# Optimization experiments

Hardware: AMD Instinct MI355X
Metric: run time of the kernel (lower is better)

## Reference

```python
import jax, jax.numpy as jnp
import numpy as np

H = 100  # hidden_size
D = 300  # input/output feature dim (hardcoded in module)
T = 32768  # number of timesteps


def _lstm_layer(x_seq, W_ih, W_hh, b_ih, b_hh):
    """Single LSTM layer over time. x_seq: [T, H_in]. PyTorch gate order i,f,g,o."""
    Hh = W_hh.shape[1]
    b = b_ih + b_hh
    # precompute input projection for all timesteps (removes per-step GEMM)
    x_proj = x_seq @ W_ih.T + b  # [T, 4H]

    def step(carry, xp_t):
        h, c = carry
        gates = xp_t + h @ W_hh.T  # [4H]
        i, f, g, o = jnp.split(gates, 4, axis=-1)
        c = jax.nn.sigmoid(f) * c + jax.nn.sigmoid(i) * jnp.tanh(g)
        h = jax.nn.sigmoid(o) * jnp.tanh(c)
        return (h, c), h

    h0 = jnp.zeros((Hh,), x_seq.dtype)
    c0 = jnp.zeros((Hh,), x_seq.dtype)
    (h_T, c_T), hs = jax.lax.scan(step, (h0, c0), x_proj)
    return hs, h_T, c_T


def setup_inputs() -> dict:
    key = jax.random.key(0)
    ks = jax.random.split(key, 14)
    s = 0.08
    return {
        "inputs": jax.random.normal(ks[0], (T, D), jnp.float32),
        "W_inp": jax.random.normal(ks[1], (H, D), jnp.float32) * s,
        "b_inp": jax.random.normal(ks[2], (H,), jnp.float32) * s,
        "W_ih_l0": jax.random.normal(ks[3], (4 * H, H), jnp.float32) * s,
        "W_hh_l0": jax.random.normal(ks[4], (4 * H, H), jnp.float32) * s,
        "b_ih_l0": jax.random.normal(ks[5], (4 * H,), jnp.float32) * s,
        "b_hh_l0": jax.random.normal(ks[6], (4 * H,), jnp.float32) * s,
        "W_ih_l1": jax.random.normal(ks[7], (4 * H, H), jnp.float32) * s,
        "W_hh_l1": jax.random.normal(ks[8], (4 * H, H), jnp.float32) * s,
        "b_ih_l1": jax.random.normal(ks[9], (4 * H,), jnp.float32) * s,
        "b_hh_l1": jax.random.normal(ks[10], (4 * H,), jnp.float32) * s,
        "W_out": jax.random.normal(ks[11], (D, H), jnp.float32) * s,
        "b_out": jax.random.normal(ks[12], (D,), jnp.float32) * s,
    }


def reference(inputs, W_inp, b_inp, W_ih_l0, W_hh_l0, b_ih_l0, b_hh_l0,
              W_ih_l1, W_hh_l1, b_ih_l1, b_hh_l1, W_out, b_out):
    # teacher-forced forward (force=True): input projection for all steps at once
    x = inputs @ W_inp.T + b_inp  # [T, H]
    h0_seq, h0_T, c0_T = _lstm_layer(x, W_ih_l0, W_hh_l0, b_ih_l0, b_hh_l0)
    h1_seq, h1_T, c1_T = _lstm_layer(h0_seq, W_ih_l1, W_hh_l1, b_ih_l1, b_hh_l1)
    outputs = h1_seq @ W_out.T + b_out  # [T, D]
    h_n = jnp.stack([h0_T, h1_T])  # [2, H] final hidden per layer
    c_n = jnp.stack([c0_T, c1_T])  # [2, H] final cell per layer
    return outputs, h_n, c_n
```

## Files before the change

kernel.cpp:

```cpp
#include <hip/hip_runtime.h>

#define T_STEPS 32768
#define OUT_BASE 9830400
#define RMASK 16383

typedef _Float16 h2 __attribute__((ext_vector_type(2)));
#define H2BC(f_) __builtin_bit_cast(h2, f_)

#define ALD(p)     __hip_atomic_load((p), __ATOMIC_RELAXED, __HIP_MEMORY_SCOPE_AGENT)
#define AST(p, v)  __hip_atomic_store((p), (v), __ATOMIC_RELAXED, __HIP_MEMORY_SCOPE_AGENT)
#define ASTR(p, v) __hip_atomic_store((p), (v), __ATOMIC_RELEASE, __HIP_MEMORY_SCOPE_AGENT)
#define CFENCE()   asm volatile("" ::: "memory")

__device__ __forceinline__ float fdot2(h2 a, h2 b, float c) {
#if __has_builtin(__builtin_amdgcn_fdot2)
    return __builtin_amdgcn_fdot2(a, b, c, false);
#else
    return c + (float)a.x * (float)b.x + (float)a.y * (float)b.y;
#endif
}

__device__ __forceinline__ float sigf(float x) { return 1.f / (1.f + __expf(-x)); }

__device__ __forceinline__ float tanh_f(float x) {
    float a = fabsf(x);
    float e = __expf(-2.f * a);
    float t = (1.f - e) / (1.f + e);
    return x < 0.f ? -t : t;
}

template <int CTRL>
__device__ __forceinline__ float qperm(float x) {
#if __has_builtin(__builtin_amdgcn_update_dpp)
    return __builtin_bit_cast(
        float, __builtin_amdgcn_update_dpp(0, __builtin_bit_cast(int, x), CTRL, 0xF, 0xF, true));
#else
    return __shfl_xor(x, CTRL == 0xB1 ? 1 : (CTRL == 0x4E ? 2 : 3));
#endif
}

__device__ __forceinline__ void bar_lds() {
    asm volatile("s_waitcnt lgkmcnt(0)\n\ts_barrier" ::: "memory");
}

__device__ __forceinline__ void ldw(h2* w, const float* p) {
#pragma unroll
    for (int k = 0; k < 25; k++) {
        float2 v = ((const float2*)p)[k];
        h2 t; t.x = (_Float16)v.x; t.y = (_Float16)v.y; w[k] = t;
    }
}

__device__ __forceinline__ float2 mv25(const h2* wA, const h2* wB, const char* rec) {
    const float4* hv = (const float4*)rec;
    float pA = 0.f, pB = 0.f;
#pragma unroll
    for (int c = 0; c < 6; c++) {
        float4 v = hv[c];
        pA = fdot2(wA[4 * c + 0], H2BC(v.x), pA); pB = fdot2(wB[4 * c + 0], H2BC(v.x), pB);
        pA = fdot2(wA[4 * c + 1], H2BC(v.y), pA); pB = fdot2(wB[4 * c + 1], H2BC(v.y), pB);
        pA = fdot2(wA[4 * c + 2], H2BC(v.z), pA); pB = fdot2(wB[4 * c + 2], H2BC(v.z), pB);
        pA = fdot2(wA[4 * c + 3], H2BC(v.w), pA); pB = fdot2(wB[4 * c + 3], H2BC(v.w), pB);
    }
    float vl = *(const float*)(rec + 96);
    pA = fdot2(wA[24], H2BC(vl), pA); pB = fdot2(wB[24], H2BC(vl), pB);
    return make_float2(pA, pB);
}

__global__ void k_precomp(const float* __restrict__ W_inp, const float* __restrict__ b_inp,
                          const float* __restrict__ W_ih0, const float* __restrict__ b_ih0,
                          const float* __restrict__ b_hh0,
                          float* __restrict__ Wc, float* __restrict__ bc) {
    int idx = blockIdx.x * 256 + threadIdx.x;
    if (idx < 120000) {
        int r = idx / 300, d = idx % 300;
        float acc = 0.f;
        for (int h = 0; h < 100; h++) acc += W_ih0[r * 100 + h] * W_inp[h * 300 + d];
        Wc[idx] = acc;
    } else if (idx < 120400) {
        int r = idx - 120000;
        float acc = b_ih0[r] + b_hh0[r];
        for (int h = 0; h < 100; h++) acc += W_ih0[r * 100 + h] * b_inp[h];
        bc[r] = acc;
    }
}

__global__ __launch_bounds__(512) void k_xproj(const float* __restrict__ inp,
                                               const float* __restrict__ Wc,
                                               const float* __restrict__ bc,
                                               _Float16* __restrict__ x0p) {
    __shared__ float xs[32 * 300];
    int t0 = blockIdx.x * 32;
    for (int idx = threadIdx.x; idx < 9600; idx += 512) xs[idx] = inp[(size_t)t0 * 300 + idx];
    __syncthreads();
    int j = threadIdx.x;
    if (j < 400) {
        float acc[32];
#pragma unroll
        for (int i = 0; i < 32; i++) acc[i] = 0.f;
        const float4* w4 = (const float4*)(Wc + j * 300);
        const float4* x4 = (const float4*)xs;
        for (int d4 = 0; d4 < 75; d4++) {
            float4 w = w4[d4];
#pragma unroll
            for (int ti = 0; ti < 32; ti++) {
                float4 x = x4[ti * 75 + d4];
                acc[ti] += w.x * x.x + w.y * x.y + w.z * x.z + w.w * x.w;
            }
        }
        float bb = bc[j];
        int dst = (j % 100) * 4 + j / 100;
#pragma unroll
        for (int ti = 0; ti < 32; ti++)
            x0p[(size_t)(t0 + ti) * 400 + dst] = (_Float16)(acc[ti] + bb);
    }
}


#define B0TICK(T_, XR_, P_) do {                                                             \
    if (j < 400) {                                                                           \
        float xc_ = XR_;                                                                     \
        int tn_ = (T_) + 2 < T_STEPS ? (T_) + 2 : T_STEPS - 1;                               \
        XR_ = (float)x0p[(size_t)tn_ * 400 + j];                                             \
        float2 p_ = mv25(wA, wB, (const char*)(lds + (P_) * 112) + hoff);                    \
        float pA_ = p_.x + qperm<0xB1>(p_.x);                                                \
        float pB_ = p_.y + qperm<0xB1>(p_.y);                                                \
        float sv_ = (H ? pB_ : pA_) + xc_;                                                   \
        float nl_ = __builtin_fmaf(sigf(sv_ * s_), s_, addc_);                               \
        float fg_ = qperm<0xB1>(nl_), gg_ = qperm<0x4E>(nl_), og_ = qperm<0x1B>(nl_);        \
        if (q == 0) {                                                                        \
            c0 = fg_ * c0 + nl_ * gg_;                                                       \
            float h0v_ = og_ * tanh_f(c0);                                                   \
            ((_Float16*)(lds + (1 - (P_)) * 112))[hidx] = (_Float16)h0v_;                    \
            if ((T_) == T_STEPS - 1) { outTail[u] = h0v_; outTail[200 + u] = c0; }           \
        }                                                                                    \
    } else if (j >= 448) {                                                                   \
        if (kk < 50 && (T_) >= 1)                                                            \
            AST(&h0seq[(size_t)((T_) - 1) * 50 + kk], (lds + (P_) * 112)[pidx]);             \
        if (kk == 0 && (((T_) & 7) == 7)) ASTR(&flags[0], (unsigned)(T_));                   \
    }                                                                                        \
    bar_lds();                                                                               \
} while (0)

#define B2TICK(T_, ZR_, P_) do {                                                             \
    if (j < 400) {                                                                           \
        float zc_ = ZR_;                                                                     \
        int tn_ = (T_) + 2 < T_STEPS ? (T_) + 2 : T_STEPS - 1;                               \
        ZR_ = ALD(&z1ring[(size_t)(tn_ & RMASK) * 400 + j]);                                 \
        float2 p_ = mv25(wA, wB, (const char*)(lds + (P_) * 112) + hoff);                    \
        float pA_ = p_.x + qperm<0xB1>(p_.x);                                                \
        float pB_ = p_.y + qperm<0xB1>(p_.y);                                                \
        float sv_ = (H ? pB_ : pA_) + zc_;              \
        float nl_ = __builtin_fmaf(sigf(sv_ * s_), s_, addc_);                               \
        float fg_ = qperm<0xB1>(nl_), gg_ = qperm<0x4E>(nl_), og_ = qperm<0x1B>(nl_);        \
        if (q == 0) {                                                                        \
            c1 = fg_ * c1 + nl_ * gg_;                                                       \
            float h1v_ = og_ * tanh_f(c1);                                                   \
            ((_Float16*)(lds + (1 - (P_)) * 112))[hidx] = (_Float16)h1v_;                    \
            h1s[(size_t)(T_) * 100 + u] = h1v_;                                              \
            if ((T_) == T_STEPS - 1) { outTail[100 + u] = h1v_; outTail[300 + u] = c1; }     \
        }                                                                                    \
    } else if (j == 448) {                                                                   \
        int tq_ = (T_) + 3 < T_STEPS ? (T_) + 3 : T_STEPS - 1;                               \
        unsigned need_ = (unsigned)(tq_ >> 4) + 1u;                                          \
        if (zdc < need_) {                                                                   \
            while ((zdc = ALD(&flags[1])) < need_) __builtin_amdgcn_s_sleep(2);              \
            CFENCE();                                                                        \
        }                                                                                    \
        if (((T_) & 255) == 255) ASTR(&flags[2], (unsigned)(T_) + 1u);                       \
    }                                                                                        \
    bar_lds();                                                                               \
} while (0)

__global__ __launch_bounds__(512) __attribute__((amdgpu_waves_per_eu(2, 2)))
void k_scan3(const _Float16* __restrict__ x0p,
             const float* __restrict__ Whh0,
             const float* __restrict__ Wih1,
             const float* __restrict__ Whh1,
             const float* __restrict__ bih1,
             const float* __restrict__ bhh1,
             float* __restrict__ h1s,
             float* __restrict__ outTail,
             unsigned* __restrict__ h0seq,
             float* __restrict__ z1ring,
             unsigned* __restrict__ flags) {
    __shared__ __align__(16) unsigned lds[16 * 56];
    const int j = threadIdx.x;
    const int q = j & 3, u = j >> 2, H = q & 1, gA = (q >> 1) * 2;
    const int hoff = H * 112;
    const int hidx = (u < 50) ? u : 56 + (u - 50);
    const int kk = j - 448;
    const int pidx = (kk < 25) ? kk : kk + 3;
    const float s_ = (q == 2) ? 2.f : 1.f;
    const float addc_ = (q == 2) ? -1.f : 0.f;

    if (blockIdx.x == 0) {
        h2 wA[25], wB[25];
        float xa = 0.f, xb = 0.f, c0 = 0.f;
        if (j < 400) {
            int r0 = gA * 100 + u;
            ldw(wA, Whh0 + r0 * 100 + 50 * H);
            ldw(wB, Whh0 + (r0 + 100) * 100 + 50 * H);
            xa = (float)x0p[j];
            xb = (float)x0p[400 + j];
        }
        if (j < 224) lds[j] = 0u;
        __syncthreads();

        for (int t = 0; t < T_STEPS; t += 2) {
            B0TICK(t, xa, 0);
            B0TICK(t + 1, xb, 1);
        }
        if (j >= 448) {
            if (kk < 50) AST(&h0seq[(size_t)(T_STEPS - 1) * 50 + kk], lds[pidx]);
            if (kk == 0) ASTR(&flags[0], (unsigned)T_STEPS);
        }
    } else if (blockIdx.x == 1) {
        h2 wA[25], wB[25];
        float bz = 0.f;
        if (j < 400) {
            int r0 = gA * 100 + u;
            ldw(wA, Wih1 + r0 * 100 + 50 * H);
            ldw(wB, Wih1 + (r0 + 100) * 100 + 50 * H);
            int ro = q * 100 + u;
            bz = bih1[ro] + bhh1[ro];
        }
        for (int idx = j; idx < 16 * 56; idx += 512) lds[idx] = 0u;
        __syncthreads();

        unsigned fcache = 0, bpc = 0;
        for (int tau = 0; tau < 2048; ++tau) {
            const int t0 = tau * 16;
            while (fcache < (unsigned)(t0 + 16)) {
                fcache = ALD(&flags[0]);
                if (fcache < (unsigned)(t0 + 16)) __builtin_amdgcn_s_sleep(8);
            }
            int lim = t0 + 32 - (RMASK + 1);
            if (lim > 0) {
                while ((int)bpc < lim) {
                    bpc = ALD(&flags[2]);
                    if ((int)bpc < lim) __builtin_amdgcn_s_sleep(8);
                }
            }
            CFENCE();
            for (int g = j; g < 800; g += 512) {
                int tt = g / 50, k = g % 50;
                lds[tt * 56 + ((k < 25) ? k : k + 3)] = ALD(&h0seq[(size_t)t0 * 50 + g]);
            }
            __syncthreads();
            if (j < 400) {
                for (int tt = 0; tt < 16; ++tt) {
                    float2 p = mv25(wA, wB, (const char*)(lds + tt * 56) + hoff);
                    float pA = p.x + qperm<0xB1>(p.x);
                    float pB = p.y + qperm<0xB1>(p.y);
                    AST(&z1ring[(size_t)((t0 + tt) & RMASK) * 400 + j], (H ? pB : pA) + bz);
                }
            }
            __syncthreads();
            if (j == 0) ASTR(&flags[1], (unsigned)(tau + 1));
        }
    } else {
        h2 wA[25], wB[25];
        float za = 0.f, zb = 0.f, c1 = 0.f;
        unsigned zdc = 0;
        if (j < 400) {
            int r0 = gA * 100 + u;
            ldw(wA, Whh1 + r0 * 100 + 50 * H);
            ldw(wB, Whh1 + (r0 + 100) * 100 + 50 * H);
        }
        if (j < 224) lds[j] = 0u;
        __syncthreads();
        if (j == 448) {
            while ((zdc = ALD(&flags[1])) < 1u) __builtin_amdgcn_s_sleep(8);
            CFENCE();
        }
        __syncthreads();
        if (j < 400) {
            za = ALD(&z1ring[j]);
            zb = ALD(&z1ring[400 + j]);
        }

        for (int t = 0; t < T_STEPS; t += 2) {
            B2TICK(t, za, 0);
            B2TICK(t + 1, zb, 1);
        }
    }
}

__global__ __launch_bounds__(320) void k_out(const float* __restrict__ h1s,
                                             const float* __restrict__ Wout,
                                             const float* __restrict__ bout,
                                             float* __restrict__ out) {
    __shared__ float hs[32 * 100];
    int t0 = blockIdx.x * 32;
    for (int idx = threadIdx.x; idx < 3200; idx += 320) hs[idx] = h1s[(size_t)t0 * 100 + idx];
    __syncthreads();
    int d = threadIdx.x;
    if (d < 300) {
        float acc[32];
#pragma unroll
        for (int i = 0; i < 32; i++) acc[i] = 0.f;
        const float4* w4 = (const float4*)(Wout + d * 100);
        const float4* h4 = (const float4*)hs;
        for (int j4 = 0; j4 < 25; j4++) {
            float4 w = w4[j4];
#pragma unroll
            for (int ti = 0; ti < 32; ti++) {
                float4 h = h4[ti * 25 + j4];
                acc[ti] += w.x * h.x + w.y * h.y + w.z * h.z + w.w * h.w;
            }
        }
        float bb = bout[d];
#pragma unroll
        for (int ti = 0; ti < 32; ti++) out[(size_t)(t0 + ti) * 300 + d] = acc[ti] + bb;
    }
}

extern "C" void kernel_launch(void* const* d_in, const int* in_sizes, int n_in,
                              void* d_out, int out_size, void* d_ws, size_t ws_size,
                              hipStream_t stream) {
    const float* inputs = (const float*)d_in[0];
    const float* W_inp  = (const float*)d_in[1];
    const float* b_inp  = (const float*)d_in[2];
    const float* W_ih0  = (const float*)d_in[3];
    const float* W_hh0  = (const float*)d_in[4];
    const float* b_ih0  = (const float*)d_in[5];
    const float* b_hh0  = (const float*)d_in[6];
    const float* W_ih1  = (const float*)d_in[7];
    const float* W_hh1  = (const float*)d_in[8];
    const float* b_ih1  = (const float*)d_in[9];
    const float* b_hh1  = (const float*)d_in[10];
    const float* W_out  = (const float*)d_in[11];
    const float* b_out  = (const float*)d_in[12];
    float* out = (float*)d_out;

    char* ws = (char*)d_ws;
    _Float16* x0p = (_Float16*)ws;
    float* h1s = (float*)(ws + 26214400);
    float* Wc  = (float*)(ws + 26214400 + 13107200);
    float* bc  = Wc + 120000;

    float*    z1ring = out;
    unsigned* h0seq  = (unsigned*)((char*)out + 26214400);
    unsigned* flagsp = (unsigned*)((char*)out + 32768000);
    float*    outTail = out + OUT_BASE;

    hipMemsetAsync(flagsp, 0, 16, stream);
    k_precomp<<<471, 256, 0, stream>>>(W_inp, b_inp, W_ih0, b_ih0, b_hh0, Wc, bc);
    k_xproj<<<1024, 512, 0, stream>>>(inputs, Wc, bc, x0p);

    void* args[] = {(void*)&x0p, (void*)&W_hh0, (void*)&W_ih1, (void*)&W_hh1,
                    (void*)&b_ih1, (void*)&b_hh1, (void*)&h1s, (void*)&outTail,
                    (void*)&h0seq, (void*)&z1ring, (void*)&flagsp};
    hipLaunchCooperativeKernel((void*)k_scan3, dim3(3), dim3(512), args, 0, stream);

    k_out<<<1024, 320, 0, stream>>>(h1s, W_out, b_out, out);
}
```

Before: 20.73 ms.

## Spread recurrent matvec over 800 threads with one gate row per thread

Each of the three scan blocks grows from 512 to 896 threads, so every thread computes half of a single gate row instead of half of two rows. This halves the serial fdot2 chain per thread on the latency-bound recurrent step and splits each dot into two accumulators. The gate lanes are regathered with new DPP permutes, including a row-rotate control. The cost is more waves per barrier, extra cross-lane shuffles, and dropping the waves-per-EU hint.

Result: slower. 26.29 ms (+26.8%).

```diff
diff --git a/kernel.cpp b/kernel.cpp
--- a/kernel.cpp
+++ b/kernel.cpp
@@ -35,7 +35,7 @@
     return __builtin_bit_cast(
         float, __builtin_amdgcn_update_dpp(0, __builtin_bit_cast(int, x), CTRL, 0xF, 0xF, true));
 #else
-    return __shfl_xor(x, CTRL == 0xB1 ? 1 : (CTRL == 0x4E ? 2 : 3));
+    return __shfl_xor(x, CTRL == 0xB1 ? 1 : (CTRL == 0x4E ? 2 : (CTRL == 0x1B ? 3 : 7)));
 #endif
 }
 
@@ -51,20 +51,20 @@
     }
 }
 
-__device__ __forceinline__ float2 mv25(const h2* wA, const h2* wB, const char* rec) {
+__device__ __forceinline__ float mv25s(const h2* w, const char* rec) {
     const float4* hv = (const float4*)rec;
-    float pA = 0.f, pB = 0.f;
+    float a0 = 0.f, a1 = 0.f;
 #pragma unroll
     for (int c = 0; c < 6; c++) {
         float4 v = hv[c];
-        pA = fdot2(wA[4 * c + 0], H2BC(v.x), pA); pB = fdot2(wB[4 * c + 0], H2BC(v.x), pB);
-        pA = fdot2(wA[4 * c + 1], H2BC(v.y), pA); pB = fdot2(wB[4 * c + 1], H2BC(v.y), pB);
-        pA = fdot2(wA[4 * c + 2], H2BC(v.z), pA); pB = fdot2(wB[4 * c + 2], H2BC(v.z), pB);
-        pA = fdot2(wA[4 * c + 3], H2BC(v.w), pA); pB = fdot2(wB[4 * c + 3], H2BC(v.w), pB);
+        a0 = fdot2(w[4 * c + 0], H2BC(v.x), a0);
+        a1 = fdot2(w[4 * c + 1], H2BC(v.y), a1);
+        a0 = fdot2(w[4 * c + 2], H2BC(v.z), a0);
+        a1 = fdot2(w[4 * c + 3], H2BC(v.w), a1);
     }
     float vl = *(const float*)(rec + 96);
-    pA = fdot2(wA[24], H2BC(vl), pA); pB = fdot2(wB[24], H2BC(vl), pB);
-    return make_float2(pA, pB);
+    a0 = fdot2(w[24], H2BC(vl), a0);
+    return a0 + a1;
 }
 
 __global__ void k_precomp(const float* __restrict__ W_inp, const float* __restrict__ b_inp,
@@ -118,23 +118,24 @@
 
 
 #define B0TICK(T_, XR_, P_) do {                                                             \
-    if (j < 400) {                                                                           \
+    if (j < 800) {                                                                           \
         float xc_ = XR_;                                                                     \
         int tn_ = (T_) + 2 < T_STEPS ? (T_) + 2 : T_STEPS - 1;                               \
-        XR_ = (float)x0p[(size_t)tn_ * 400 + j];                                             \
-        float2 p_ = mv25(wA, wB, (const char*)(lds + (P_) * 112) + hoff);                    \
-        float pA_ = p_.x + qperm<0xB1>(p_.x);                                                \
-        float pB_ = p_.y + qperm<0xB1>(p_.y);                                                \
-        float sv_ = (H ? pB_ : pA_) + xc_;                                                   \
-        float nl_ = __builtin_fmaf(sigf(sv_ * s_), s_, addc_);                               \
-        float fg_ = qperm<0xB1>(nl_), gg_ = qperm<0x4E>(nl_), og_ = qperm<0x1B>(nl_);        \
-        if (q == 0) {                                                                        \
+        XR_ = (float)x0p[(size_t)tn_ * 400 + (j >> 1)];                                      \
+        float s_v = mv25s(w, (const char*)(lds + (P_) * 112) + hoff);                        \
+        s_v += qperm<0xB1>(s_v);                                                             \
+        s_v += xc_;                                                                          \
+        float nl_ = __builtin_fmaf(sigf(s_v * s_), s_, addc_);                               \
+        float fg_ = qperm<0x4E>(nl_);                                                        \
+        float og_ = qperm<0x141>(nl_);                                                       \
+        float gg_ = qperm<0x141>(qperm<0x1B>(nl_));                                          \
+        if ((j & 7) == 0) {                                                                  \
             c0 = fg_ * c0 + nl_ * gg_;                                                       \
             float h0v_ = og_ * tanh_f(c0);                                                   \
             ((_Float16*)(lds + (1 - (P_)) * 112))[hidx] = (_Float16)h0v_;                    \
             if ((T_) == T_STEPS - 1) { outTail[u] = h0v_; outTail[200 + u] = c0; }           \
         }                                                                                    \
-    } else if (j >= 448) {                                                                   \
+    } else if (j >= 832) {                                                                   \
         if (kk < 50 && (T_) >= 1)                                                            \
             AST(&h0seq[(size_t)((T_) - 1) * 50 + kk], (lds + (P_) * 112)[pidx]);             \
         if (kk == 0 && (((T_) & 7) == 7)) ASTR(&flags[0], (unsigned)(T_));                   \
@@ -143,24 +144,25 @@
 } while (0)
 
 #define B2TICK(T_, ZR_, P_) do {                                                             \
-    if (j < 400) {                                                                           \
+    if (j < 800) {                                                                           \
         float zc_ = ZR_;                                                                     \
         int tn_ = (T_) + 2 < T_STEPS ? (T_) + 2 : T_STEPS - 1;                               \
-        ZR_ = ALD(&z1ring[(size_t)(tn_ & RMASK) * 400 + j]);                                 \
-        float2 p_ = mv25(wA, wB, (const char*)(lds + (P_) * 112) + hoff);                    \
-        float pA_ = p_.x + qperm<0xB1>(p_.x);                                                \
-        float pB_ = p_.y + qperm<0xB1>(p_.y);                                                \
-        float sv_ = (H ? pB_ : pA_) + zc_;              \
-        float nl_ = __builtin_fmaf(sigf(sv_ * s_), s_, addc_);                               \
-        float fg_ = qperm<0xB1>(nl_), gg_ = qperm<0x4E>(nl_), og_ = qperm<0x1B>(nl_);        \
-        if (q == 0) {                                                                        \
+        ZR_ = ALD(&z1ring[(size_t)(tn_ & RMASK) * 400 + (j >> 1)]);                          \
+        float s_v = mv25s(w, (const char*)(lds + (P_) * 112) + hoff);                        \
+        s_v += qperm<0xB1>(s_v);                                                             \
+        s_v += zc_;                                     \
+        float nl_ = __builtin_fmaf(sigf(s_v * s_), s_, addc_);                               \
+        float fg_ = qperm<0x4E>(nl_);                                                        \
+        float og_ = qperm<0x141>(nl_);                                                       \
+        float gg_ = qperm<0x141>(qperm<0x1B>(nl_));                                          \
+        if ((j & 7) == 0) {                                                                  \
             c1 = fg_ * c1 + nl_ * gg_;                                                       \
             float h1v_ = og_ * tanh_f(c1);                                                   \
             ((_Float16*)(lds + (1 - (P_)) * 112))[hidx] = (_Float16)h1v_;                    \
             h1s[(size_t)(T_) * 100 + u] = h1v_;                                              \
             if ((T_) == T_STEPS - 1) { outTail[100 + u] = h1v_; outTail[300 + u] = c1; }     \
         }                                                                                    \
-    } else if (j == 448) {                                                                   \
+    } else if (j == 832) {                                                                   \
         int tq_ = (T_) + 3 < T_STEPS ? (T_) + 3 : T_STEPS - 1;                               \
         unsigned need_ = (unsigned)(tq_ >> 4) + 1u;                                          \
         if (zdc < need_) {                                                                   \
@@ -172,7 +174,7 @@
     bar_lds();                                                                               \
 } while (0)
 
-__global__ __launch_bounds__(512) __attribute__((amdgpu_waves_per_eu(2, 2)))
+__global__ __launch_bounds__(896)
 void k_scan3(const _Float16* __restrict__ x0p,
              const float* __restrict__ Whh0,
              const float* __restrict__ Wih1,
@@ -186,23 +188,22 @@
              unsigned* __restrict__ flags) {
     __shared__ __align__(16) unsigned lds[16 * 56];
     const int j = threadIdx.x;
-    const int q = j & 3, u = j >> 2, H = q & 1, gA = (q >> 1) * 2;
+    const int q = (j >> 1) & 3, u = j >> 3, H = j & 1;
     const int hoff = H * 112;
     const int hidx = (u < 50) ? u : 56 + (u - 50);
-    const int kk = j - 448;
+    const int kk = j - 832;
     const int pidx = (kk < 25) ? kk : kk + 3;
     const float s_ = (q == 2) ? 2.f : 1.f;
     const float addc_ = (q == 2) ? -1.f : 0.f;
 
     if (blockIdx.x == 0) {
-        h2 wA[25], wB[25];
+        h2 w[25];
         float xa = 0.f, xb = 0.f, c0 = 0.f;
-        if (j < 400) {
-            int r0 = gA * 100 + u;
-            ldw(wA, Whh0 + r0 * 100 + 50 * H);
-            ldw(wB, Whh0 + (r0 + 100) * 100 + 50 * H);
-            xa = (float)x0p[j];
-            xb = (float)x0p[400 + j];
+        if (j < 800) {
+            int r = q * 100 + u;
+            ldw(w, Whh0 + r * 100 + 50 * H);
+            xa = (float)x0p[j >> 1];
+            xb = (float)x0p[400 + (j >> 1)];
         }
         if (j < 224) lds[j] = 0u;
         __syncthreads();
@@ -211,21 +212,19 @@
             B0TICK(t, xa, 0);
             B0TICK(t + 1, xb, 1);
         }
-        if (j >= 448) {
+        if (j >= 832) {
             if (kk < 50) AST(&h0seq[(size_t)(T_STEPS - 1) * 50 + kk], lds[pidx]);
             if (kk == 0) ASTR(&flags[0], (unsigned)T_STEPS);
         }
     } else if (blockIdx.x == 1) {
-        h2 wA[25], wB[25];
+        h2 w[25];
         float bz = 0.f;
-        if (j < 400) {
-            int r0 = gA * 100 + u;
-            ldw(wA, Wih1 + r0 * 100 + 50 * H);
-            ldw(wB, Wih1 + (r0 + 100) * 100 + 50 * H);
-            int ro = q * 100 + u;
-            bz = bih1[ro] + bhh1[ro];
-        }
-        for (int idx = j; idx < 16 * 56; idx += 512) lds[idx] = 0u;
+        if (j < 800) {
+            int r = q * 100 + u;
+            ldw(w, Wih1 + r * 100 + 50 * H);
+            bz = bih1[r] + bhh1[r];
+        }
+        for (int idx = j; idx < 16 * 56; idx += 896) lds[idx] = 0u;
         __syncthreads();
 
         unsigned fcache = 0, bpc = 0;
@@ -243,41 +242,40 @@
                 }
             }
             CFENCE();
-            for (int g = j; g < 800; g += 512) {
-                int tt = g / 50, k = g % 50;
-                lds[tt * 56 + ((k < 25) ? k : k + 3)] = ALD(&h0seq[(size_t)t0 * 50 + g]);
+            if (j < 800) {
+                int tt = j / 50, k = j % 50;
+                lds[tt * 56 + ((k < 25) ? k : k + 3)] = ALD(&h0seq[(size_t)t0 * 50 + j]);
             }
             __syncthreads();
-            if (j < 400) {
+            if (j < 800) {
                 for (int tt = 0; tt < 16; ++tt) {
-                    float2 p = mv25(wA, wB, (const char*)(lds + tt * 56) + hoff);
-                    float pA = p.x + qperm<0xB1>(p.x);
-                    float pB = p.y + qperm<0xB1>(p.y);
-                    AST(&z1ring[(size_t)((t0 + tt) & RMASK) * 400 + j], (H ? pB : pA) + bz);
+                    float s_v = mv25s(w, (const char*)(lds + tt * 56) + hoff);
+                    s_v += qperm<0xB1>(s_v);
+                    if (H == 0)
+                        AST(&z1ring[(size_t)((t0 + tt) & RMASK) * 400 + (j >> 1)], s_v + bz);
                 }
             }
             __syncthreads();
             if (j == 0) ASTR(&flags[1], (unsigned)(tau + 1));
         }
     } else {
-        h2 wA[25], wB[25];
+        h2 w[25];
         float za = 0.f, zb = 0.f, c1 = 0.f;
         unsigned zdc = 0;
-        if (j < 400) {
-            int r0 = gA * 100 + u;
-            ldw(wA, Whh1 + r0 * 100 + 50 * H);
-            ldw(wB, Whh1 + (r0 + 100) * 100 + 50 * H);
+        if (j < 800) {
+            int r = q * 100 + u;
+            ldw(w, Whh1 + r * 100 + 50 * H);
         }
         if (j < 224) lds[j] = 0u;
         __syncthreads();
-        if (j == 448) {
+        if (j == 832) {
             while ((zdc = ALD(&flags[1])) < 1u) __builtin_amdgcn_s_sleep(8);
             CFENCE();
         }
         __syncthreads();
-        if (j < 400) {
-            za = ALD(&z1ring[j]);
-            zb = ALD(&z1ring[400 + j]);
+        if (j < 800) {
+            za = ALD(&z1ring[j >> 1]);
+            zb = ALD(&z1ring[400 + (j >> 1)]);
         }
 
         for (int t = 0; t < T_STEPS; t += 2) {
@@ -352,7 +350,7 @@
     void* args[] = {(void*)&x0p, (void*)&W_hh0, (void*)&W_ih1, (void*)&W_hh1,
                     (void*)&b_ih1, (void*)&b_hh1, (void*)&h1s, (void*)&outTail,
                     (void*)&h0seq, (void*)&z1ring, (void*)&flagsp};
-    hipLaunchCooperativeKernel((void*)k_scan3, dim3(3), dim3(512), args, 0, stream);
+    hipLaunchCooperativeKernel((void*)k_scan3, dim3(3), dim3(896), args, 0, stream);
 
     k_out<<<1024, 320, 0, stream>>>(h1s, W_out, b_out, out);
 }
```

## Split hidden dimension across quad lanes with all four gates per lane

Applied to the files above, without the earlier changes.

The recurrent matvec is re-partitioned. Each quad of lanes now owns one hidden unit, and each lane covers a quarter of the hidden vector (13 h2 pairs) for all four gates, instead of two gates over half the vector. Partial sums are combined with a two-stage DPP butterfly, so every lane ends up holding all four gate preactivations and computes the cell update locally, replacing the earlier gate-exchange permutes. The LDS layout for h changes to 16-element-padded quarter segments, and x0p is kept in half precision in registers. This is meant to shorten the serial per-step critical path, at the cost of redundant nonlinearity work across the four lanes.

Measured after the change: 27.02 ms. +30.4%, slower.

```diff
diff --git a/kernel.cpp b/kernel.cpp
--- a/kernel.cpp
+++ b/kernel.cpp
@@ -35,7 +35,7 @@
     return __builtin_bit_cast(
         float, __builtin_amdgcn_update_dpp(0, __builtin_bit_cast(int, x), CTRL, 0xF, 0xF, true));
 #else
-    return __shfl_xor(x, CTRL == 0xB1 ? 1 : (CTRL == 0x4E ? 2 : 3));
+    return __shfl_xor(x, CTRL == 0xB1 ? 1 : 2);
 #endif
 }
 
@@ -43,29 +43,49 @@
     asm volatile("s_waitcnt lgkmcnt(0)\n\ts_barrier" ::: "memory");
 }
 
-__device__ __forceinline__ void ldw(h2* w, const float* p) {
-#pragma unroll
-    for (int k = 0; k < 25; k++) {
-        float2 v = ((const float2*)p)[k];
-        h2 t; t.x = (_Float16)v.x; t.y = (_Float16)v.y; w[k] = t;
-    }
-}
-
-__device__ __forceinline__ float2 mv25(const h2* wA, const h2* wB, const char* rec) {
-    const float4* hv = (const float4*)rec;
-    float pA = 0.f, pB = 0.f;
-#pragma unroll
-    for (int c = 0; c < 6; c++) {
-        float4 v = hv[c];
-        pA = fdot2(wA[4 * c + 0], H2BC(v.x), pA); pB = fdot2(wB[4 * c + 0], H2BC(v.x), pB);
-        pA = fdot2(wA[4 * c + 1], H2BC(v.y), pA); pB = fdot2(wB[4 * c + 1], H2BC(v.y), pB);
-        pA = fdot2(wA[4 * c + 2], H2BC(v.z), pA); pB = fdot2(wB[4 * c + 2], H2BC(v.z), pB);
-        pA = fdot2(wA[4 * c + 3], H2BC(v.w), pA); pB = fdot2(wB[4 * c + 3], H2BC(v.w), pB);
-    }
-    float vl = *(const float*)(rec + 96);
-    pA = fdot2(wA[24], H2BC(vl), pA); pB = fdot2(wB[24], H2BC(vl), pB);
-    return make_float2(pA, pB);
-}
+__device__ __forceinline__ void ldw13(h2* w, const float* rowp, int sg) {
+    const float2* p = (const float2*)(rowp + 26 * sg);
+    int n = (sg == 3) ? 11 : 13;
+    for (int k = 0; k < 13; k++) {
+        h2 t;
+        if (k < n) { float2 v = p[k]; t.x = (_Float16)v.x; t.y = (_Float16)v.y; }
+        else       { t.x = (_Float16)0.f; t.y = (_Float16)0.f; }
+        w[k] = t;
+    }
+}
+
+#define MVQ(REC_)                                                                            \
+    float s0_, s1_, s2_, s3_;                                                                \
+    {                                                                                        \
+        const char* sp_ = (const char*)(REC_) + (sg << 6);                                   \
+        float4 v0_ = *(const float4*)sp_;                                                    \
+        float4 v1_ = *(const float4*)(sp_ + 16);                                             \
+        float4 v2_ = *(const float4*)(sp_ + 32);                                             \
+        float  v3_ = *(const float*)(sp_ + 48);                                              \
+        h2 hs_[13] = {H2BC(v0_.x), H2BC(v0_.y), H2BC(v0_.z), H2BC(v0_.w),                    \
+                      H2BC(v1_.x), H2BC(v1_.y), H2BC(v1_.z), H2BC(v1_.w),                    \
+                      H2BC(v2_.x), H2BC(v2_.y), H2BC(v2_.z), H2BC(v2_.w),                    \
+                      H2BC(v3_)};                                                            \
+        float a_[4], b_[4];                                                                  \
+        _Pragma("unroll") for (int g_ = 0; g_ < 4; g_++) { a_[g_] = 0.f; b_[g_] = 0.f; }     \
+        _Pragma("unroll") for (int k_ = 0; k_ < 12; k_ += 2) {                               \
+            _Pragma("unroll") for (int g_ = 0; g_ < 4; g_++) {                               \
+                a_[g_] = fdot2(w[g_][k_],     hs_[k_],     a_[g_]);                          \
+                b_[g_] = fdot2(w[g_][k_ + 1], hs_[k_ + 1], b_[g_]);                          \
+            }                                                                                \
+        }                                                                                    \
+        _Pragma("unroll") for (int g_ = 0; g_ < 4; g_++)                                     \
+            a_[g_] = fdot2(w[g_][12], hs_[12], a_[g_]);                                      \
+        s0_ = a_[0] + b_[0]; s1_ = a_[1] + b_[1];                                            \
+        s2_ = a_[2] + b_[2]; s3_ = a_[3] + b_[3];                                            \
+    }
+
+#define BFLY4() do {                                                                         \
+    s0_ += qperm<0xB1>(s0_); s1_ += qperm<0xB1>(s1_);                                        \
+    s2_ += qperm<0xB1>(s2_); s3_ += qperm<0xB1>(s3_);                                        \
+    s0_ += qperm<0x4E>(s0_); s1_ += qperm<0x4E>(s1_);                                        \
+    s2_ += qperm<0x4E>(s2_); s3_ += qperm<0x4E>(s3_);                                        \
+} while (0)
 
 __global__ void k_precomp(const float* __restrict__ W_inp, const float* __restrict__ b_inp,
                           const float* __restrict__ W_ih0, const float* __restrict__ b_ih0,
@@ -119,24 +139,23 @@
 
 #define B0TICK(T_, XR_, P_) do {                                                             \
     if (j < 400) {                                                                           \
-        float xc_ = XR_;                                                                     \
+        float xf_ = (float)XR_;                                                              \
         int tn_ = (T_) + 2 < T_STEPS ? (T_) + 2 : T_STEPS - 1;                               \
-        XR_ = (float)x0p[(size_t)tn_ * 400 + j];                                             \
-        float2 p_ = mv25(wA, wB, (const char*)(lds + (P_) * 112) + hoff);                    \
-        float pA_ = p_.x + qperm<0xB1>(p_.x);                                                \
-        float pB_ = p_.y + qperm<0xB1>(p_.y);                                                \
-        float sv_ = (H ? pB_ : pA_) + xc_;                                                   \
-        float nl_ = __builtin_fmaf(sigf(sv_ * s_), s_, addc_);                               \
-        float fg_ = qperm<0xB1>(nl_), gg_ = qperm<0x4E>(nl_), og_ = qperm<0x1B>(nl_);        \
-        if (q == 0) {                                                                        \
-            c0 = fg_ * c0 + nl_ * gg_;                                                       \
-            float h0v_ = og_ * tanh_f(c0);                                                   \
-            ((_Float16*)(lds + (1 - (P_)) * 112))[hidx] = (_Float16)h0v_;                    \
-            if ((T_) == T_STEPS - 1) { outTail[u] = h0v_; outTail[200 + u] = c0; }           \
+        XR_ = x0p[(size_t)tn_ * 400 + j];                                                    \
+        MVQ(lds + (P_) * 64);                                                                \
+        s0_ = __builtin_fmaf(m0, xf_, s0_); s1_ = __builtin_fmaf(m1, xf_, s1_);              \
+        s2_ = __builtin_fmaf(m2, xf_, s2_); s3_ = __builtin_fmaf(m3, xf_, s3_);              \
+        BFLY4();                                                                             \
+        float si_ = sigf(s0_), sf_ = sigf(s1_), tg_ = tanh_f(s2_), so_ = sigf(s3_);          \
+        c0 = sf_ * c0 + si_ * tg_;                                                           \
+        float hv_ = so_ * tanh_f(c0);                                                        \
+        if (sg == 0) {                                                                       \
+            ((_Float16*)(lds + (1 - (P_)) * 64))[hpos] = (_Float16)hv_;                      \
+            if ((T_) == T_STEPS - 1) { outTail[u] = hv_; outTail[200 + u] = c0; }            \
         }                                                                                    \
     } else if (j >= 448) {                                                                   \
         if (kk < 50 && (T_) >= 1)                                                            \
-            AST(&h0seq[(size_t)((T_) - 1) * 50 + kk], (lds + (P_) * 112)[pidx]);             \
+            AST(&h0seq[(size_t)((T_) - 1) * 50 + kk], (lds + (P_) * 64)[hp2]);               \
         if (kk == 0 && (((T_) & 7) == 7)) ASTR(&flags[0], (unsigned)(T_));                   \
     }                                                                                        \
     bar_lds();                                                                               \
@@ -144,21 +163,20 @@
 
 #define B2TICK(T_, ZR_, P_) do {                                                             \
     if (j < 400) {                                                                           \
-        float zc_ = ZR_;                                                                     \
+        float zf_ = ZR_;                                                                     \
         int tn_ = (T_) + 2 < T_STEPS ? (T_) + 2 : T_STEPS - 1;                               \
         ZR_ = ALD(&z1ring[(size_t)(tn_ & RMASK) * 400 + j]);                                 \
-        float2 p_ = mv25(wA, wB, (const char*)(lds + (P_) * 112) + hoff);                    \
-        float pA_ = p_.x + qperm<0xB1>(p_.x);                                                \
-        float pB_ = p_.y + qperm<0xB1>(p_.y);                                                \
-        float sv_ = (H ? pB_ : pA_) + zc_;              \
-        float nl_ = __builtin_fmaf(sigf(sv_ * s_), s_, addc_);                               \
-        float fg_ = qperm<0xB1>(nl_), gg_ = qperm<0x4E>(nl_), og_ = qperm<0x1B>(nl_);        \
-        if (q == 0) {                                                                        \
-            c1 = fg_ * c1 + nl_ * gg_;                                                       \
-            float h1v_ = og_ * tanh_f(c1);                                                   \
-            ((_Float16*)(lds + (1 - (P_)) * 112))[hidx] = (_Float16)h1v_;                    \
-            h1s[(size_t)(T_) * 100 + u] = h1v_;                                              \
-            if ((T_) == T_STEPS - 1) { outTail[100 + u] = h1v_; outTail[300 + u] = c1; }     \
+        MVQ(lds + (P_) * 64);                                                                \
+        s0_ = __builtin_fmaf(m0, zf_, s0_); s1_ = __builtin_fmaf(m1, zf_, s1_);              \
+        s2_ = __builtin_fmaf(m2, zf_, s2_); s3_ = __builtin_fmaf(m3, zf_, s3_);              \
+        BFLY4();                                                                             \
+        float si_ = sigf(s0_), sf_ = sigf(s1_), tg_ = tanh_f(s2_), so_ = sigf(s3_);          \
+        c1 = sf_ * c1 + si_ * tg_;                                                           \
+        float hv_ = so_ * tanh_f(c1);                                                        \
+        if (sg == 0) {                                                                       \
+            ((_Float16*)(lds + (1 - (P_)) * 64))[hpos] = (_Float16)hv_;                      \
+            h1s[(size_t)(T_) * 100 + u] = hv_;                                               \
+            if ((T_) == T_STEPS - 1) { outTail[100 + u] = hv_; outTail[300 + u] = c1; }      \
         }                                                                                    \
     } else if (j == 448) {                                                                   \
         int tq_ = (T_) + 3 < T_STEPS ? (T_) + 3 : T_STEPS - 1;                               \
@@ -184,27 +202,27 @@
              unsigned* __restrict__ h0seq,
              float* __restrict__ z1ring,
              unsigned* __restrict__ flags) {
-    __shared__ __align__(16) unsigned lds[16 * 56];
+    __shared__ __align__(16) unsigned lds[1024];
     const int j = threadIdx.x;
-    const int q = j & 3, u = j >> 2, H = q & 1, gA = (q >> 1) * 2;
-    const int hoff = H * 112;
-    const int hidx = (u < 50) ? u : 56 + (u - 50);
+    const int u = (j >> 2), sg = j & 3;
+    const int hpos = (u / 26) * 32 + (u % 26);
     const int kk = j - 448;
-    const int pidx = (kk < 25) ? kk : kk + 3;
-    const float s_ = (q == 2) ? 2.f : 1.f;
-    const float addc_ = (q == 2) ? -1.f : 0.f;
+    const int e2 = 2 * (kk < 0 ? 0 : (kk > 49 ? 49 : kk));
+    const int hp2 = (e2 / 26) * 16 + (e2 % 26) / 2;
+    const float m0 = (sg == 0) ? 1.f : 0.f, m1 = (sg == 1) ? 1.f : 0.f;
+    const float m2 = (sg == 2) ? 1.f : 0.f, m3 = (sg == 3) ? 1.f : 0.f;
 
     if (blockIdx.x == 0) {
-        h2 wA[25], wB[25];
-        float xa = 0.f, xb = 0.f, c0 = 0.f;
+        h2 w[4][13];
+        _Float16 xa = (_Float16)0.f, xb = (_Float16)0.f;
+        float c0 = 0.f;
         if (j < 400) {
-            int r0 = gA * 100 + u;
-            ldw(wA, Whh0 + r0 * 100 + 50 * H);
-            ldw(wB, Whh0 + (r0 + 100) * 100 + 50 * H);
-            xa = (float)x0p[j];
-            xb = (float)x0p[400 + j];
-        }
-        if (j < 224) lds[j] = 0u;
+#pragma unroll
+            for (int g = 0; g < 4; g++) ldw13(w[g], Whh0 + (g * 100 + u) * 100, sg);
+            xa = x0p[j];
+            xb = x0p[400 + j];
+        }
+        if (j < 128) lds[j] = 0u;
         __syncthreads();
 
         for (int t = 0; t < T_STEPS; t += 2) {
@@ -212,20 +230,19 @@
             B0TICK(t + 1, xb, 1);
         }
         if (j >= 448) {
-            if (kk < 50) AST(&h0seq[(size_t)(T_STEPS - 1) * 50 + kk], lds[pidx]);
+            if (kk < 50) AST(&h0seq[(size_t)(T_STEPS - 1) * 50 + kk], lds[hp2]);
             if (kk == 0) ASTR(&flags[0], (unsigned)T_STEPS);
         }
     } else if (blockIdx.x == 1) {
-        h2 wA[25], wB[25];
+        h2 w[4][13];
         float bz = 0.f;
         if (j < 400) {
-            int r0 = gA * 100 + u;
-            ldw(wA, Wih1 + r0 * 100 + 50 * H);
-            ldw(wB, Wih1 + (r0 + 100) * 100 + 50 * H);
-            int ro = q * 100 + u;
+#pragma unroll
+            for (int g = 0; g < 4; g++) ldw13(w[g], Wih1 + (g * 100 + u) * 100, sg);
+            int ro = sg * 100 + u;
             bz = bih1[ro] + bhh1[ro];
         }
-        for (int idx = j; idx < 16 * 56; idx += 512) lds[idx] = 0u;
+        for (int idx = j; idx < 1024; idx += 512) lds[idx] = 0u;
         __syncthreads();
 
         unsigned fcache = 0, bpc = 0;
@@ -245,30 +262,34 @@
             CFENCE();
             for (int g = j; g < 800; g += 512) {
                 int tt = g / 50, k = g % 50;
-                lds[tt * 56 + ((k < 25) ? k : k + 3)] = ALD(&h0seq[(size_t)t0 * 50 + g]);
+                int e = 2 * k;
+                lds[tt * 64 + (e / 26) * 16 + (e % 26) / 2] =
+                    ALD(&h0seq[(size_t)t0 * 50 + g]);
             }
             __syncthreads();
             if (j < 400) {
                 for (int tt = 0; tt < 16; ++tt) {
-                    float2 p = mv25(wA, wB, (const char*)(lds + tt * 56) + hoff);
-                    float pA = p.x + qperm<0xB1>(p.x);
-                    float pB = p.y + qperm<0xB1>(p.y);
-                    AST(&z1ring[(size_t)((t0 + tt) & RMASK) * 400 + j], (H ? pB : pA) + bz);
+                    MVQ(lds + tt * 64);
+                    s0_ = __builtin_fmaf(m0, bz, s0_); s1_ = __builtin_fmaf(m1, bz, s1_);
+                    s2_ = __builtin_fmaf(m2, bz, s2_); s3_ = __builtin_fmaf(m3, bz, s3_);
+                    BFLY4();
+                    float zo_ = sg == 0 ? s0_ : (sg == 1 ? s1_ : (sg == 2 ? s2_ : s3_));
+                    AST((unsigned*)&z1ring[(size_t)((t0 + tt) & RMASK) * 400 + j],
+                        __builtin_bit_cast(unsigned, zo_));
                 }
             }
             __syncthreads();
             if (j == 0) ASTR(&flags[1], (unsigned)(tau + 1));
         }
     } else {
-        h2 wA[25], wB[25];
+        h2 w[4][13];
         float za = 0.f, zb = 0.f, c1 = 0.f;
         unsigned zdc = 0;
         if (j < 400) {
-            int r0 = gA * 100 + u;
-            ldw(wA, Whh1 + r0 * 100 + 50 * H);
-            ldw(wB, Whh1 + (r0 + 100) * 100 + 50 * H);
-        }
-        if (j < 224) lds[j] = 0u;
+#pragma unroll
+            for (int g = 0; g < 4; g++) ldw13(w[g], Whh1 + (g * 100 + u) * 100, sg);
+        }
+        if (j < 128) lds[j] = 0u;
         __syncthreads();
         if (j == 448) {
             while ((zdc = ALD(&flags[1])) < 1u) __builtin_amdgcn_s_sleep(8);
@@ -276,8 +297,8 @@
         }
         __syncthreads();
         if (j < 400) {
-            za = ALD(&z1ring[j]);
-            zb = ALD(&z1ring[400 + j]);
+            za = __builtin_bit_cast(float, ALD((const unsigned*)&z1ring[j]));
+            zb = __builtin_bit_cast(float, ALD((const unsigned*)&z1ring[400 + j]));
         }
 
         for (int t = 0; t < T_STEPS; t += 2) {
```

## Use MFMA 16x16x32 f16 for recurrent matvec in both LSTM scan blocks

Applied to the files above, without the earlier changes.

Replaces the per-thread fdot2 recurrent matvec in the layer-0 and layer-1 scan blocks with MFMA 16x16x32 f16 chains. Each wave holds packed W_hh tiles in registers and reads h from LDS as the B operand. Gate rows are interleaved so that each lane receives i,f,g,o for one hidden unit, which removes the DPP gate shuffles. The intent is to shorten the serial per-timestep critical path. The cost is MFMA latency on a matvec where only one B column is useful, extra per-lane selects, and a changed LDS layout for h.

Measured after the change: 26.88 ms. +29.7%, slower.

```diff
diff --git a/kernel.cpp b/kernel.cpp
--- a/kernel.cpp
+++ b/kernel.cpp
@@ -5,12 +5,16 @@
 #define RMASK 16383
 
 typedef _Float16 h2 __attribute__((ext_vector_type(2)));
+typedef _Float16 f16x8 __attribute__((ext_vector_type(8)));
+typedef float f32x4 __attribute__((ext_vector_type(4)));
 #define H2BC(f_) __builtin_bit_cast(h2, f_)
 
 #define ALD(p)     __hip_atomic_load((p), __ATOMIC_RELAXED, __HIP_MEMORY_SCOPE_AGENT)
 #define AST(p, v)  __hip_atomic_store((p), (v), __ATOMIC_RELAXED, __HIP_MEMORY_SCOPE_AGENT)
 #define ASTR(p, v) __hip_atomic_store((p), (v), __ATOMIC_RELEASE, __HIP_MEMORY_SCOPE_AGENT)
 #define CFENCE()   asm volatile("" ::: "memory")
+
+#define MFMA16(A_, B_, C_) __builtin_amdgcn_mfma_f32_16x16x32_f16(A_, B_, C_, 0, 0, 0)
 
 __device__ __forceinline__ float fdot2(h2 a, h2 b, float c) {
 #if __has_builtin(__builtin_amdgcn_fdot2)
@@ -35,7 +39,7 @@
     return __builtin_bit_cast(
         float, __builtin_amdgcn_update_dpp(0, __builtin_bit_cast(int, x), CTRL, 0xF, 0xF, true));
 #else
-    return __shfl_xor(x, CTRL == 0xB1 ? 1 : (CTRL == 0x4E ? 2 : 3));
+    return __shfl_xor(x, 1);
 #endif
 }
 
@@ -65,6 +69,28 @@
     float vl = *(const float*)(rec + 96);
     pA = fdot2(wA[24], H2BC(vl), pA); pB = fdot2(wB[24], H2BC(vl), pB);
     return make_float2(pA, pB);
+}
+
+__device__ __forceinline__ void packA(f16x8* wf, const float* W, int tile, int col, int grp) {
+    int rp = 16 * tile + col;
+    const float* wr = W + ((rp & 3) * 100 + (rp >> 2)) * 100;
+#pragma unroll
+    for (int kt = 0; kt < 4; kt++) {
+        f16x8 a;
+#pragma unroll
+        for (int jj = 0; jj < 8; jj++) {
+            int k = kt * 32 + grp * 8 + jj;
+            a[jj] = (k < 100) ? (_Float16)wr[k] : (_Float16)0.f;
+        }
+        wf[kt] = a;
+    }
+}
+
+__device__ __forceinline__ f32x4 xcvt(unsigned long long v) {
+    h2 p0 = __builtin_bit_cast(h2, (unsigned)(v & 0xffffffffu));
+    h2 p1 = __builtin_bit_cast(h2, (unsigned)(v >> 32));
+    f32x4 r; r[0] = (float)p0.x; r[1] = (float)p0.y; r[2] = (float)p1.x; r[3] = (float)p1.y;
+    return r;
 }
 
 __global__ void k_precomp(const float* __restrict__ W_inp, const float* __restrict__ b_inp,
@@ -117,59 +143,33 @@
 }
 
 
-#define B0TICK(T_, XR_, P_) do {                                                             \
-    if (j < 400) {                                                                           \
-        float xc_ = XR_;                                                                     \
-        int tn_ = (T_) + 2 < T_STEPS ? (T_) + 2 : T_STEPS - 1;                               \
-        XR_ = (float)x0p[(size_t)tn_ * 400 + j];                                             \
-        float2 p_ = mv25(wA, wB, (const char*)(lds + (P_) * 112) + hoff);                    \
-        float pA_ = p_.x + qperm<0xB1>(p_.x);                                                \
-        float pB_ = p_.y + qperm<0xB1>(p_.y);                                                \
-        float sv_ = (H ? pB_ : pA_) + xc_;                                                   \
-        float nl_ = __builtin_fmaf(sigf(sv_ * s_), s_, addc_);                               \
-        float fg_ = qperm<0xB1>(nl_), gg_ = qperm<0x4E>(nl_), og_ = qperm<0x1B>(nl_);        \
-        if (q == 0) {                                                                        \
-            c0 = fg_ * c0 + nl_ * gg_;                                                       \
-            float h0v_ = og_ * tanh_f(c0);                                                   \
-            ((_Float16*)(lds + (1 - (P_)) * 112))[hidx] = (_Float16)h0v_;                    \
-            if ((T_) == T_STEPS - 1) { outTail[u] = h0v_; outTail[200 + u] = c0; }           \
-        }                                                                                    \
-    } else if (j >= 448) {                                                                   \
-        if (kk < 50 && (T_) >= 1)                                                            \
-            AST(&h0seq[(size_t)((T_) - 1) * 50 + kk], (lds + (P_) * 112)[pidx]);             \
-        if (kk == 0 && (((T_) & 7) == 7)) ASTR(&flags[0], (unsigned)(T_));                   \
-    }                                                                                        \
-    bar_lds();                                                                               \
+#define CHAIN4(ACC_, WF_) do {                                                               \
+    ACC_ = MFMA16(WF_[0], hf0, ACC_); ACC_ = MFMA16(WF_[1], hf1, ACC_);                      \
+    ACC_ = MFMA16(WF_[2], hf2, ACC_); ACC_ = MFMA16(WF_[3], hf3, ACC_);                      \
 } while (0)
 
-#define B2TICK(T_, ZR_, P_) do {                                                             \
-    if (j < 400) {                                                                           \
-        float zc_ = ZR_;                                                                     \
-        int tn_ = (T_) + 2 < T_STEPS ? (T_) + 2 : T_STEPS - 1;                               \
-        ZR_ = ALD(&z1ring[(size_t)(tn_ & RMASK) * 400 + j]);                                 \
-        float2 p_ = mv25(wA, wB, (const char*)(lds + (P_) * 112) + hoff);                    \
-        float pA_ = p_.x + qperm<0xB1>(p_.x);                                                \
-        float pB_ = p_.y + qperm<0xB1>(p_.y);                                                \
-        float sv_ = (H ? pB_ : pA_) + zc_;              \
-        float nl_ = __builtin_fmaf(sigf(sv_ * s_), s_, addc_);                               \
-        float fg_ = qperm<0xB1>(nl_), gg_ = qperm<0x4E>(nl_), og_ = qperm<0x1B>(nl_);        \
-        if (q == 0) {                                                                        \
-            c1 = fg_ * c1 + nl_ * gg_;                                                       \
-            float h1v_ = og_ * tanh_f(c1);                                                   \
-            ((_Float16*)(lds + (1 - (P_)) * 112))[hidx] = (_Float16)h1v_;                    \
-            h1s[(size_t)(T_) * 100 + u] = h1v_;                                              \
-            if ((T_) == T_STEPS - 1) { outTail[100 + u] = h1v_; outTail[300 + u] = c1; }     \
-        }                                                                                    \
-    } else if (j == 448) {                                                                   \
-        int tq_ = (T_) + 3 < T_STEPS ? (T_) + 3 : T_STEPS - 1;                               \
-        unsigned need_ = (unsigned)(tq_ >> 4) + 1u;                                          \
-        if (zdc < need_) {                                                                   \
-            while ((zdc = ALD(&flags[1])) < need_) __builtin_amdgcn_s_sleep(2);              \
-            CFENCE();                                                                        \
-        }                                                                                    \
-        if (((T_) & 255) == 255) ASTR(&flags[2], (unsigned)(T_) + 1u);                       \
-    }                                                                                        \
-    bar_lds();                                                                               \
+#define SCAN_CORE(P_, CI0_, CI1_, CI2_, CI3_, CS_, HV_) do {                                 \
+    const char* rb_ = (const char*)lds + (P_) * 256;                                         \
+    f16x8 hf0 = *(const f16x8*)(rb_ + grp * 16);                                             \
+    f16x8 hf1 = *(const f16x8*)(rb_ + 64 + grp * 16);                                        \
+    f16x8 hf2 = *(const f16x8*)(rb_ + 128 + grp * 16);                                       \
+    f16x8 hf3 = *(const f16x8*)(rb_ + 192 + grp * 16);                                       \
+    f32x4 a0_ = CI0_, a1_ = CI1_, a2_ = CI2_;                                                \
+    CHAIN4(a0_, w0); CHAIN4(a1_, w1); CHAIN4(a2_, w2);                                       \
+    f32x4 gv_;                                                                               \
+    if (wid == 0) {                                                                          \
+        f32x4 a3_ = CI3_;                                                                    \
+        CHAIN4(a3_, w3);                                                                     \
+        gv_ = (lsel == 0) ? a0_ : ((lsel == 1) ? a1_ : ((lsel == 2) ? a2_ : a3_));           \
+    } else {                                                                                 \
+        gv_ = (lsel == 0) ? a0_ : ((lsel == 1) ? a1_ : a2_);                                 \
+    }                                                                                        \
+    float si_ = sigf(gv_[0]), sf_ = sigf(gv_[1]);                                            \
+    float tg_ = tanh_f(gv_[2]), so_ = sigf(gv_[3]);                                          \
+    CS_ = sf_ * CS_ + si_ * tg_;                                                             \
+    HV_ = so_ * tanh_f(CS_);                                                                 \
+    if ((l & 15) < 4)                                                                        \
+        ((_Float16*)((char*)lds + (1 - (P_)) * 256))[uS] = (_Float16)HV_;                    \
 } while (0)
 
 __global__ __launch_bounds__(512) __attribute__((amdgpu_waves_per_eu(2, 2)))
@@ -184,38 +184,70 @@
              unsigned* __restrict__ h0seq,
              float* __restrict__ z1ring,
              unsigned* __restrict__ flags) {
-    __shared__ __align__(16) unsigned lds[16 * 56];
+    __shared__ __align__(16) unsigned lds[896];
     const int j = threadIdx.x;
-    const int q = j & 3, u = j >> 2, H = q & 1, gA = (q >> 1) * 2;
-    const int hoff = H * 112;
-    const int hidx = (u < 50) ? u : 56 + (u - 50);
-    const int kk = j - 448;
-    const int pidx = (kk < 25) ? kk : kk + 3;
-    const float s_ = (q == 2) ? 2.f : 1.f;
-    const float addc_ = (q == 2) ? -1.f : 0.f;
 
     if (blockIdx.x == 0) {
-        h2 wA[25], wB[25];
-        float xa = 0.f, xb = 0.f, c0 = 0.f;
-        if (j < 400) {
-            int r0 = gA * 100 + u;
-            ldw(wA, Whh0 + r0 * 100 + 50 * H);
-            ldw(wB, Whh0 + (r0 + 100) * 100 + 50 * H);
-            xa = (float)x0p[j];
-            xb = (float)x0p[400 + j];
-        }
-        if (j < 224) lds[j] = 0u;
+        const int wid = j >> 6, l = j & 63, col = l & 15, grp = l >> 4, lsel = l & 3;
+        const int t0_ = wid, t1_ = wid + 8, t2_ = wid + 16;
+        const int uD0 = 4 * t0_ + grp, uD1 = 4 * t1_ + grp, uD2 = 4 * t2_ + grp;
+        const int uD3 = 96 + grp;
+        int tsel;
+        if (wid == 0) tsel = (lsel == 0) ? t0_ : ((lsel == 1) ? t1_ : ((lsel == 2) ? t2_ : 24));
+        else          tsel = (lsel == 0) ? t0_ : ((lsel == 1) ? t1_ : t2_);
+        const int uS = 4 * tsel + grp;
+
+        f16x8 w0[4], w1[4], w2[4], w3[4];
+        packA(w0, Whh0, t0_, col, grp);
+        packA(w1, Whh0, t1_, col, grp);
+        packA(w2, Whh0, t2_, col, grp);
+        packA(w3, Whh0, (wid == 0) ? 24 : t2_, col, grp);
+
+        unsigned long long XA0, XA1, XA2, XA3, XB0, XB1, XB2, XB3;
+        XA0 = *(const unsigned long long*)(x0p + 4 * uD0);
+        XA1 = *(const unsigned long long*)(x0p + 4 * uD1);
+        XA2 = *(const unsigned long long*)(x0p + 4 * uD2);
+        XA3 = *(const unsigned long long*)(x0p + 4 * uD3);
+        XB0 = *(const unsigned long long*)(x0p + 400 + 4 * uD0);
+        XB1 = *(const unsigned long long*)(x0p + 400 + 4 * uD1);
+        XB2 = *(const unsigned long long*)(x0p + 400 + 4 * uD2);
+        XB3 = *(const unsigned long long*)(x0p + 400 + 4 * uD3);
+
+        if (j < 128) lds[j] = 0u;
+        float c0 = 0.f, hv = 0.f;
         __syncthreads();
 
+#define B0TICK(T_, P_, X0_, X1_, X2_, X3_) do {                                              \
+    f32x4 ci0_ = xcvt(X0_), ci1_ = xcvt(X1_), ci2_ = xcvt(X2_), ci3_ = xcvt(X3_);            \
+    {                                                                                        \
+        int tn_ = (T_) + 2 < T_STEPS ? (T_) + 2 : T_STEPS - 1;                               \
+        const _Float16* xb_ = x0p + (size_t)tn_ * 400;                                       \
+        X0_ = *(const unsigned long long*)(xb_ + 4 * uD0);                                   \
+        X1_ = *(const unsigned long long*)(xb_ + 4 * uD1);                                   \
+        X2_ = *(const unsigned long long*)(xb_ + 4 * uD2);                                   \
+        X3_ = *(const unsigned long long*)(xb_ + 4 * uD3);                                   \
+    }                                                                                        \
+    SCAN_CORE(P_, ci0_, ci1_, ci2_, ci3_, c0, hv);                                           \
+    if ((T_) == T_STEPS - 1 && (l & 15) < 4) { outTail[uS] = hv; outTail[200 + uS] = c0; }   \
+    if (wid == 7 && l < 50) {                                                                \
+        if ((T_) >= 1) AST(&h0seq[(size_t)((T_) - 1) * 50 + l], lds[(P_) * 64 + l]);         \
+        if (l == 0 && (((T_) & 7) == 7)) ASTR(&flags[0], (unsigned)(T_));                    \
+    }                                                                                        \
+    bar_lds();                                                                               \
+} while (0)
+
         for (int t = 0; t < T_STEPS; t += 2) {
-            B0TICK(t, xa, 0);
-            B0TICK(t + 1, xb, 1);
-        }
-        if (j >= 448) {
-            if (kk < 50) AST(&h0seq[(size_t)(T_STEPS - 1) * 50 + kk], lds[pidx]);
-            if (kk == 0) ASTR(&flags[0], (unsigned)T_STEPS);
-        }
+            B0TICK(t, 0, XA0, XA1, XA2, XA3);
+            B0TICK(t + 1, 1, XB0, XB1, XB2, XB3);
+        }
+        if (wid == 7 && l < 50) {
+            AST(&h0seq[(size_t)(T_STEPS - 1) * 50 + l], lds[l]);
+            if (l == 0) ASTR(&flags[0], (unsigned)T_STEPS);
+        }
+#undef B0TICK
     } else if (blockIdx.x == 1) {
+        const int q = j & 3, u = j >> 2, H = q & 1, gA = (q >> 1) * 2;
+        const int hoff = H * 112;
         h2 wA[25], wB[25];
         float bz = 0.f;
         if (j < 400) {
@@ -225,7 +257,7 @@
             int ro = q * 100 + u;
             bz = bih1[ro] + bhh1[ro];
         }
-        for (int idx = j; idx < 16 * 56; idx += 512) lds[idx] = 0u;
+        for (int idx = j; idx < 896; idx += 512) lds[idx] = 0u;
         __syncthreads();
 
         unsigned fcache = 0, bpc = 0;
@@ -253,37 +285,80 @@
                     float2 p = mv25(wA, wB, (const char*)(lds + tt * 56) + hoff);
                     float pA = p.x + qperm<0xB1>(p.x);
                     float pB = p.y + qperm<0xB1>(p.y);
-                    AST(&z1ring[(size_t)((t0 + tt) & RMASK) * 400 + j], (H ? pB : pA) + bz);
+                    AST((unsigned*)&z1ring[(size_t)((t0 + tt) & RMASK) * 400 + j],
+                        __builtin_bit_cast(unsigned, (H ? pB : pA) + bz));
                 }
             }
             __syncthreads();
             if (j == 0) ASTR(&flags[1], (unsigned)(tau + 1));
         }
     } else {
-        h2 wA[25], wB[25];
-        float za = 0.f, zb = 0.f, c1 = 0.f;
+        const int wid = j >> 6, l = j & 63, col = l & 15, grp = l >> 4, lsel = l & 3;
+        const int t0_ = wid, t1_ = wid + 8, t2_ = wid + 16;
+        const int uD0 = 4 * t0_ + grp, uD1 = 4 * t1_ + grp, uD2 = 4 * t2_ + grp;
+        const int uD3 = 96 + grp;
+        int tsel;
+        if (wid == 0) tsel = (lsel == 0) ? t0_ : ((lsel == 1) ? t1_ : ((lsel == 2) ? t2_ : 24));
+        else          tsel = (lsel == 0) ? t0_ : ((lsel == 1) ? t1_ : t2_);
+        const int uS = 4 * tsel + grp;
+
+        f16x8 w0[4], w1[4], w2[4], w3[4];
+        packA(w0, Whh1, t0_, col, grp);
+        packA(w1, Whh1, t1_, col, grp);
+        packA(w2, Whh1, t2_, col, grp);
+        packA(w3, Whh1, (wid == 0) ? 24 : t2_, col, grp);
+
+        if (j < 128) lds[j] = 0u;
+        float c1 = 0.f, hv = 0.f;
         unsigned zdc = 0;
-        if (j < 400) {
-            int r0 = gA * 100 + u;
-            ldw(wA, Whh1 + r0 * 100 + 50 * H);
-            ldw(wB, Whh1 + (r0 + 100) * 100 + 50 * H);
-        }
-        if (j < 224) lds[j] = 0u;
         __syncthreads();
         if (j == 448) {
             while ((zdc = ALD(&flags[1])) < 1u) __builtin_amdgcn_s_sleep(8);
             CFENCE();
         }
         __syncthreads();
-        if (j < 400) {
-            za = ALD(&z1ring[j]);
-            zb = ALD(&z1ring[400 + j]);
-        }
+
+        f32x4 ZA0, ZA1, ZA2, ZA3, ZB0, ZB1, ZB2, ZB3;
+#define ZLOAD(D_, TK_, UD_) do {                                                             \
+    const unsigned* zp_ = (const unsigned*)z1ring + (size_t)((TK_) & RMASK) * 400 + 4 * (UD_);\
+    D_[0] = __builtin_bit_cast(float, ALD(zp_ + 0));                                         \
+    D_[1] = __builtin_bit_cast(float, ALD(zp_ + 1));                                         \
+    D_[2] = __builtin_bit_cast(float, ALD(zp_ + 2));                                         \
+    D_[3] = __builtin_bit_cast(float, ALD(zp_ + 3));                                         \
+} while (0)
+        ZLOAD(ZA0, 0, uD0); ZLOAD(ZA1, 0, uD1); ZLOAD(ZA2, 0, uD2); ZLOAD(ZA3, 0, uD3);
+        ZLOAD(ZB0, 1, uD0); ZLOAD(ZB1, 1, uD1); ZLOAD(ZB2, 1, uD2); ZLOAD(ZB3, 1, uD3);
+
+#define B2TICK(T_, P_, Z0_, Z1_, Z2_, Z3_) do {                                              \
+    f32x4 ci0_ = Z0_, ci1_ = Z1_, ci2_ = Z2_, ci3_ = Z3_;                                    \
+    {                                                                                        \
+        int tn_ = (T_) + 2 < T_STEPS ? (T_) + 2 : T_STEPS - 1;                               \
+        ZLOAD(Z0_, tn_, uD0); ZLOAD(Z1_, tn_, uD1);                                          \
+        ZLOAD(Z2_, tn_, uD2); ZLOAD(Z3_, tn_, uD3);                                          \
+    }                                                                                        \
+    SCAN_CORE(P_, ci0_, ci1_, ci2_, ci3_, c1, hv);                                           \
+    if ((l & 15) < 4) {                                                                      \
+        h1s[(size_t)(T_) * 100 + uS] = hv;                                                   \
+        if ((T_) == T_STEPS - 1) { outTail[100 + uS] = hv; outTail[300 + uS] = c1; }         \
+    }                                                                                        \
+    if (j == 448) {                                                                          \
+        int tq_ = (T_) + 3 < T_STEPS ? (T_) + 3 : T_STEPS - 1;                               \
+        unsigned need_ = (unsigned)(tq_ >> 4) + 1u;                                          \
+        if (zdc < need_) {                                                                   \
+            while ((zdc = ALD(&flags[1])) < need_) __builtin_amdgcn_s_sleep(2);              \
+            CFENCE();                                                                        \
+        }                                                                                    \
+        if (((T_) & 255) == 255) ASTR(&flags[2], (unsigned)(T_) + 1u);                       \
+    }                                                                                        \
+    bar_lds();                                                                               \
+} while (0)
 
         for (int t = 0; t < T_STEPS; t += 2) {
-            B2TICK(t, za, 0);
-            B2TICK(t + 1, zb, 1);
-        }
+            B2TICK(t, 0, ZA0, ZA1, ZA2, ZA3);
+            B2TICK(t + 1, 1, ZB0, ZB1, ZB2, ZB3);
+        }
+#undef B2TICK
+#undef ZLOAD
     }
 }
 
```
